# Performance work log

Hardware: AMD Instinct MI355X
Metric: run time of the kernel (lower is better)

Reference implementation:

```python
import jax, jax.numpy as jnp
import numpy as np

NUM_FEATURES = 256
NUM_HEADS = 8
HEAD_SIZE = NUM_FEATURES // NUM_HEADS  # 32
N_AGENTS = 8
B = 32
SEQ = 64


def setup_inputs() -> dict:
    key = jax.random.key(0)
    ks = jax.random.split(key, 6)
    s = 0.02
    x = jax.random.normal(ks[0], (N_AGENTS * B, NUM_FEATURES, SEQ), dtype=jnp.float32)
    Wq = jax.random.normal(ks[1], (NUM_HEADS, NUM_FEATURES, HEAD_SIZE), dtype=jnp.float32) * s
    Wk = jax.random.normal(ks[2], (NUM_HEADS, NUM_FEATURES, HEAD_SIZE), dtype=jnp.float32) * s
    Wv = jax.random.normal(ks[3], (NUM_HEADS, NUM_FEATURES, HEAD_SIZE), dtype=jnp.float32) * s
    Wp = jax.random.normal(ks[4], (NUM_FEATURES, NUM_FEATURES), dtype=jnp.float32) * s
    bp = jnp.zeros((NUM_FEATURES,), dtype=jnp.float32)
    return {"x": x, "Wq": Wq, "Wk": Wk, "Wv": Wv, "Wp": Wp, "bp": bp, "n_agents": N_AGENTS}


def reference(x, Wq, Wk, Wv, Wp, bp, n_agents):
    # x: (n_agents*b, f, h)
    b_total, f, h = x.shape
    b = b_total // n_agents
    # reshape + rearrange 'n b f h -> n b h f'  (t = token axis of length h)
    xs = x.reshape(n_agents, b, f, h).transpose(0, 1, 3, 2)  # (n, b, t, f)
    # All heads at once: per-head linear projections (no bias)
    q = jnp.einsum('nbtf,Hfd->Hnbtd', xs, Wq)
    k = jnp.einsum('nbtf,Hfd->Hnbtd', xs, Wk)
    v = jnp.einsum('nbtf,Hfd->Hnbtd', xs, Wv)
    # all-pairs agent attention: i = key agent, j = query agent
    scale = f ** (-0.5)  # source scales by num_features, not head_size
    scores = jnp.einsum('Hjbtd,Hibsd->Hijbts', q, k) * scale  # (H,n,n,b,t,s)
    attn = jax.nn.softmax(scores, axis=-1)
    # weighted values, then sum over key-agent axis i
    out = jnp.einsum('Hijbts,Hibsd->Hjbtd', attn, v)  # (H,n,b,t,d)
    # concat heads on last dim (head 0 first), matching torch.cat
    y = jnp.moveaxis(out, 0, 3).reshape(n_agents, b, h, f)  # (n,b,t,H*d)
    # output projection (dropout is identity at eval / p=0)
    y = jnp.einsum('nbtf,gf->nbtg', y, Wp) + bp
    # rearrange 'n b h f -> n b f h' then merge agents into batch
    y = y.transpose(0, 1, 3, 2).reshape(n_agents * b, f, h)
    return y
```

## Files before the change

kernel.cpp:

```cpp
#include <hip/hip_runtime.h>

#define F   256
#define T   64
#define NH  8
#define D   32
#define NA  8
#define NBB 32

typedef unsigned short ushortT;
typedef unsigned int   uintT;

typedef short bf16x8 __attribute__((ext_vector_type(8)));
typedef float f32x4  __attribute__((ext_vector_type(4)));

__device__ __forceinline__ float bf2f(ushortT u) {
    union { uintT i; float f; } c; c.i = ((uintT)u) << 16; return c.f;
}
__device__ __forceinline__ ushortT f2bf(float f) {
    union { float f; uintT u; } c; c.f = f;
    uintT u = c.u;
    uintT r = u + 0x7fffu + ((u >> 16) & 1u);
    return (ushortT)(r >> 16);
}

__device__ __forceinline__ int detect_isbf16(const void* xraw) {
    const uintT* w = (const uintT*)xraw;
    int bad = 0;
    for (int k = 0; k < 128; ++k) {
        uintT v = w[k];
        uintT e0 = (v >> 7)  & 0xffu;
        uintT e1 = (v >> 23) & 0xffu;
        bad += (e0 > 131u) + (e1 > 131u);
    }
    return bad == 0 ? 1 : 0;
}

__device__ __forceinline__ ushortT cvt_elem(const void* p, size_t i, bool isbf) {
    return isbf ? ((const ushortT*)p)[i] : f2bf(((const float*)p)[i]);
}

__device__ __forceinline__ void packc(const f32x4 v, float scale, uintT& u0, uintT& u1) {
    u0 = (uintT)f2bf(v[0] * scale) | ((uintT)f2bf(v[1] * scale) << 16);
    u1 = (uintT)f2bf(v[2] * scale) | ((uintT)f2bf(v[3] * scale) << 16);
}

__device__ __forceinline__ bf16x8 build_frag(uintT u0a, uintT u1a, uintT u0b, uintT u1b,
                                             int sl0, int sl1, bool hi) {
    union { uintT u[4]; bf16x8 v; } r;
    uintT x0a = (uintT)__shfl((int)u0a, sl0), x0b = (uintT)__shfl((int)u0b, sl0);
    uintT x1a = (uintT)__shfl((int)u1a, sl0), x1b = (uintT)__shfl((int)u1b, sl0);
    uintT x2a = (uintT)__shfl((int)u0a, sl1), x2b = (uintT)__shfl((int)u0b, sl1);
    uintT x3a = (uintT)__shfl((int)u1a, sl1), x3b = (uintT)__shfl((int)u1b, sl1);
    r.u[0] = hi ? x0b : x0a;
    r.u[1] = hi ? x1b : x1a;
    r.u[2] = hi ? x2b : x2a;
    r.u[3] = hi ? x3b : x3a;
    return r.v;
}

__device__ __forceinline__ int xposU(int t, int f) {
    return t * 256 + ((((f >> 3) ^ (t & 31)) * 8) | (f & 7));
}
#define FRAGPOS(t_, ks_, quad_) \
    ((t_) * 256 + ((((4 * (ks_) + (quad_)) ^ ((t_) & 31)) * 8)))


__global__ __launch_bounds__(256) void wprep_kernel(const void* __restrict__ Wq,
                                                    const void* __restrict__ Wk,
                                                    const void* __restrict__ Wv,
                                                    const void* __restrict__ Wp,
                                                    const void* __restrict__ x,
                                                    ushortT* __restrict__ Wt) {
    __shared__ int sflag;
    if (threadIdx.x == 0) sflag = detect_isbf16(x);
    __syncthreads();
    bool isbf = sflag != 0;

    int base = (blockIdx.x * 256 + threadIdx.x) * 8;
    int cp = base >> 8, f0 = base & 255;

    ushortT tmp[8];
    if (cp < 768) {
        int qkv = cp >> 8, c = cp & 255, hh = c >> 5, d = c & 31;
        const void* W = (qkv == 0) ? Wq : (qkv == 1) ? Wk : Wv;
        #pragma unroll
        for (int jj = 0; jj < 8; ++jj)
            tmp[jj] = cvt_elem(W, (size_t)(hh * F + f0 + jj) * D + d, isbf);
    } else {
        int g = cp - 768;
        #pragma unroll
        for (int jj = 0; jj < 8; ++jj)
            tmp[jj] = cvt_elem(Wp, (size_t)g * F + f0 + jj, isbf);
    }
    *(uint4*)&Wt[base] = *(const uint4*)tmp;
}

template <int NT>
__device__ __forceinline__ void stage_xT(const void* x, int nb, ushortT* xs,
                                         bool isbf, int tid) {
    int t = tid & 63;
    int g0 = tid >> 6;
    const int GP = NT / 64;
    #pragma unroll
    for (int it = 0; it < 64 / GP; ++it) {
        int g = g0 + it * GP;
        float v0, v1, v2, v3;
        if (isbf) {
            const ushortT* xp = (const ushortT*)x + (size_t)nb * (F * T) + (size_t)g * 4 * T + t;
            v0 = bf2f(xp[0]); v1 = bf2f(xp[T]); v2 = bf2f(xp[2 * T]); v3 = bf2f(xp[3 * T]);
        } else {
            const float* xp = (const float*)x + (size_t)nb * (F * T) + (size_t)g * 4 * T + t;
            v0 = xp[0]; v1 = xp[T]; v2 = xp[2 * T]; v3 = xp[3 * T];
        }
        uintT lo = (uintT)f2bf(v0) | ((uintT)f2bf(v1) << 16);
        uintT hi2 = (uintT)f2bf(v2) | ((uintT)f2bf(v3) << 16);
        *(uint2*)&xs[xposU(t & 31, g * 4) + (t >> 5) * 8192] = make_uint2(lo, hi2);
    }
}

__global__ __launch_bounds__(256) void qkv_kernel(const void* __restrict__ x,
                                                  const ushortT* __restrict__ Wt,
                                                  ushortT* __restrict__ Kws,
                                                  ushortT* __restrict__ Vws) {
    int nb = blockIdx.x, half = blockIdx.y;
    __shared__ __align__(16) ushortT xs[T * F];
    __shared__ int sflag;
    int tid = threadIdx.x;
    if (tid == 0) sflag = detect_isbf16(x);
    __syncthreads();
    bool isbf = sflag != 0;
    stage_xT<256>(x, nb, xs, isbf, tid);
    __syncthreads();

    int w = tid >> 6, lane = tid & 63, l15 = lane & 15, quad = lane >> 4;
    int rowbase = 256 + 256 * half + 64 * w;

    f32x4 acc[4][4];
    #pragma unroll
    for (int a = 0; a < 4; ++a)
        #pragma unroll
        for (int c = 0; c < 4; ++c) acc[a][c] = (f32x4){0.f, 0.f, 0.f, 0.f};

    #pragma unroll
    for (int ks = 0; ks < 8; ++ks) {
        bf16x8 Bfr[4];
        #pragma unroll
        for (int nt = 0; nt < 4; ++nt) {
            int t = 16 * nt + l15;
            Bfr[nt] = *(const bf16x8*)&xs[FRAGPOS(t & 31, ks, quad) + (t >> 5) * 8192];
        }
        #pragma unroll
        for (int mt = 0; mt < 4; ++mt) {
            bf16x8 Afr = *(const bf16x8*)(Wt +
                (size_t)(rowbase + 16 * mt + l15) * 256 + ks * 32 + quad * 8);
            #pragma unroll
            for (int nt = 0; nt < 4; ++nt)
                acc[mt][nt] = __builtin_amdgcn_mfma_f32_16x16x32_bf16(Afr, Bfr[nt],
                                                                      acc[mt][nt], 0, 0, 0);
        }
    }

    #pragma unroll
    for (int mt = 0; mt < 4; ++mt) {
        int rel = 64 * w + 16 * mt + 4 * quad;
        int hh = rel >> 5, db = rel & 31;
        #pragma unroll
        for (int nt = 0; nt < 4; ++nt) {
            int t = 16 * nt + l15;
            f32x4 v = acc[mt][nt];
            if (half == 0) {
                ushortT* dst = Kws + ((size_t)(nb * NH + hh) * T + t) * D + db;
                uintT lo = (uintT)f2bf(v[0]) | ((uintT)f2bf(v[1]) << 16);
                uintT hi2 = (uintT)f2bf(v[2]) | ((uintT)f2bf(v[3]) << 16);
                *(uint2*)dst = make_uint2(lo, hi2);
            } else {
                #pragma unroll
                for (int r = 0; r < 4; ++r)
                    Vws[((size_t)(nb * NH + hh) * D + db + r) * T + t] = f2bf(v[r]);
            }
        }
    }
}

__global__ __launch_bounds__(512, 2) void attn_kernel(const void* __restrict__ x,
                                                      const ushortT* __restrict__ Wt,
                                                      const ushortT* __restrict__ Kws,
                                                      const ushortT* __restrict__ Vws,
                                                      const void* __restrict__ bp,
                                                      void* __restrict__ outp) {
    __shared__ __align__(16) ushortT xs[32 * F];
    __shared__ float bpf[F];
    __shared__ int sflag;

    int tid = threadIdx.x;
    int b = blockIdx.x, j = blockIdx.y, tb = blockIdx.z;
    int nbj = j * NBB + b;

    if (tid == 0) sflag = detect_isbf16(x);
    __syncthreads();
    bool isbf = sflag != 0;

    {
        int t = tid & 31, fg = tid >> 5;
        int ta = tb * 32 + t;
        #pragma unroll
        for (int it = 0; it < 4; ++it) {
            int f0 = (fg + 16 * it) * 4;
            float v0, v1, v2, v3;
            if (isbf) {
                const ushortT* xp = (const ushortT*)x + (size_t)nbj * (F * T) +
                                    (size_t)f0 * T + ta;
                v0 = bf2f(xp[0]); v1 = bf2f(xp[T]); v2 = bf2f(xp[2 * T]); v3 = bf2f(xp[3 * T]);
            } else {
                const float* xp = (const float*)x + (size_t)nbj * (F * T) +
                                  (size_t)f0 * T + ta;
                v0 = xp[0]; v1 = xp[T]; v2 = xp[2 * T]; v3 = xp[3 * T];
            }
            uintT lo = (uintT)f2bf(v0) | ((uintT)f2bf(v1) << 16);
            uintT hi2 = (uintT)f2bf(v2) | ((uintT)f2bf(v3) << 16);
            *(uint2*)&xs[xposU(t, f0)] = make_uint2(lo, hi2);
        }
    }
    if (tid < 256)
        bpf[tid] = isbf ? bf2f(((const ushortT*)bp)[tid]) : ((const float*)bp)[tid];
    __syncthreads();

    int h = tid >> 6, lane = tid & 63, l15 = lane & 15, quad = lane >> 4;
    bool hi = quad >= 2;
    int sl0 = l15 + 32 * (quad & 1), sl1 = sl0 + 16;

    bf16x8 qf[2];
    {
        f32x4 qacc[2][2];
        #pragma unroll
        for (int mt = 0; mt < 2; ++mt)
            #pragma unroll
            for (int nt = 0; nt < 2; ++nt) qacc[mt][nt] = (f32x4){0.f, 0.f, 0.f, 0.f};
        #pragma unroll
        for (int ks = 0; ks < 8; ++ks) {
            bf16x8 xf[2];
            #pragma unroll
            for (int nt = 0; nt < 2; ++nt)
                xf[nt] = *(const bf16x8*)&xs[FRAGPOS(16 * nt + l15, ks, quad)];
            #pragma unroll
            for (int mt = 0; mt < 2; ++mt) {
                bf16x8 Aw = *(const bf16x8*)(Wt +
                    (size_t)(32 * h + 16 * mt + l15) * 256 + ks * 32 + quad * 8);
                #pragma unroll
                for (int nt = 0; nt < 2; ++nt)
                    qacc[mt][nt] = __builtin_amdgcn_mfma_f32_16x16x32_bf16(
                        Aw, xf[nt], qacc[mt][nt], 0, 0, 0);
            }
        }
        #pragma unroll
        for (int tt = 0; tt < 2; ++tt) {
            uintT a0, a1, b0, b1;
            packc(qacc[0][tt], 0.0625f, a0, a1);
            packc(qacc[1][tt], 0.0625f, b0, b1);
            qf[tt] = build_frag(a0, a1, b0, b1, sl0, sl1, hi);
        }
    }

    f32x4 oacc[2][2];
    #pragma unroll
    for (int mt = 0; mt < 2; ++mt)
        #pragma unroll
        for (int tt = 0; tt < 2; ++tt) oacc[mt][tt] = (f32x4){0.f, 0.f, 0.f, 0.f};

    for (int i = 0; i < NA; ++i) {
        int nbi = i * NBB + b;
        const ushortT* Kb = Kws + (size_t)(nbi * NH + h) * T * D;
        const ushortT* Vb = Vws + (size_t)(nbi * NH + h) * D * T;

        float psum[2] = {0.f, 0.f};
        f32x4 pv[2][2];
        #pragma unroll
        for (int mt = 0; mt < 2; ++mt)
            #pragma unroll
            for (int tt = 0; tt < 2; ++tt) pv[mt][tt] = (f32x4){0.f, 0.f, 0.f, 0.f};

        #pragma unroll
        for (int kx = 0; kx < 2; ++kx) {
            uintT pu0[2][2], pu1[2][2];
            #pragma unroll
            for (int sp = 0; sp < 2; ++sp) {
                bf16x8 kf = *(const bf16x8*)(Kb + (16 * (2 * kx + sp) + l15) * D + quad * 8);
                #pragma unroll
                for (int tt = 0; tt < 2; ++tt) {
                    f32x4 s4 = __builtin_amdgcn_mfma_f32_16x16x32_bf16(
                        kf, qf[tt], (f32x4){0.f, 0.f, 0.f, 0.f}, 0, 0, 0);
                    #pragma unroll
                    for (int r = 0; r < 4; ++r) {
                        float e = __expf(s4[r]);
                        s4[r] = e;
                        psum[tt] += e;
                    }
                    packc(s4, 1.f, pu0[sp][tt], pu1[sp][tt]);
                }
            }
            bf16x8 vf0 = *(const bf16x8*)(Vb + l15 * T + kx * 32 + quad * 8);
            bf16x8 vf1 = *(const bf16x8*)(Vb + (16 + l15) * T + kx * 32 + quad * 8);
            #pragma unroll
            for (int tt = 0; tt < 2; ++tt) {
                bf16x8 pf = build_frag(pu0[0][tt], pu1[0][tt], pu0[1][tt], pu1[1][tt],
                                       sl0, sl1, hi);
                pv[0][tt] = __builtin_amdgcn_mfma_f32_16x16x32_bf16(
                    vf0, pf, pv[0][tt], 0, 0, 0);
                pv[1][tt] = __builtin_amdgcn_mfma_f32_16x16x32_bf16(
                    vf1, pf, pv[1][tt], 0, 0, 0);
            }
        }

        #pragma unroll
        for (int tt = 0; tt < 2; ++tt) {
            float s = psum[tt];
            s += __shfl_xor(s, 16);
            s += __shfl_xor(s, 32);
            float inv = 1.0f / s;
            #pragma unroll
            for (int mt = 0; mt < 2; ++mt)
                #pragma unroll
                for (int r = 0; r < 4; ++r)
                    oacc[mt][tt][r] = fmaf(inv, pv[mt][tt][r], oacc[mt][tt][r]);
        }
    }

    __syncthreads();
    #pragma unroll
    for (int mt = 0; mt < 2; ++mt)
        #pragma unroll
        for (int tt = 0; tt < 2; ++tt) {
            int t = 16 * tt + l15;
            int cb = 32 * h + 16 * mt + 4 * quad;
            uintT u0, u1;
            packc(oacc[mt][tt], 1.f, u0, u1);
            *(uint2*)&xs[xposU(t, cb)] = make_uint2(u0, u1);
        }
    __syncthreads();

    f32x4 cacc[2][2];
    #pragma unroll
    for (int a = 0; a < 2; ++a)
        #pragma unroll
        for (int c = 0; c < 2; ++c) cacc[a][c] = (f32x4){0.f, 0.f, 0.f, 0.f};

    #pragma unroll
    for (int ks = 0; ks < 8; ++ks) {
        bf16x8 yb[2];
        #pragma unroll
        for (int nt = 0; nt < 2; ++nt)
            yb[nt] = *(const bf16x8*)&xs[FRAGPOS(16 * nt + l15, ks, quad)];
        #pragma unroll
        for (int m2 = 0; m2 < 2; ++m2) {
            int g = 16 * (2 * h + m2) + l15;
            bf16x8 wf = *(const bf16x8*)(Wt + (size_t)(768 + g) * 256 + ks * 32 + quad * 8);
            #pragma unroll
            for (int nt = 0; nt < 2; ++nt)
                cacc[m2][nt] = __builtin_amdgcn_mfma_f32_16x16x32_bf16(
                    wf, yb[nt], cacc[m2][nt], 0, 0, 0);
        }
    }

    #pragma unroll
    for (int m2 = 0; m2 < 2; ++m2)
        #pragma unroll
        for (int nt = 0; nt < 2; ++nt) {
            int t = tb * 32 + 16 * nt + l15;
            #pragma unroll
            for (int r = 0; r < 4; ++r) {
                int g = 16 * (2 * h + m2) + 4 * quad + r;
                float val = cacc[m2][nt][r] + bpf[g];
                if (isbf)
                    ((ushortT*)outp)[(size_t)nbj * F * T + g * T + t] = f2bf(val);
                else
                    ((float*)outp)[(size_t)nbj * F * T + g * T + t] = val;
            }
        }
}

__device__ __forceinline__ float tof(ushortT u) { return bf2f(u); }
__device__ __forceinline__ float tof(float f)   { return f; }

__device__ __forceinline__ void stage_x(const void* x, size_t nb, ushortT* sX,
                                        bool isbf, int tid) {
    if (isbf) {
        const int4* xg = (const int4*)((const ushortT*)x + nb * (F * T));
        int4* xl = (int4*)sX;
        for (int kk = tid; kk < F * T / 8; kk += 512) xl[kk] = xg[kk];
    } else {
        const float4* xg = (const float4*)((const float*)x + nb * (F * T));
        for (int kk = tid; kk < F * T / 4; kk += 512) {
            float4 v = xg[kk];
            int o = kk * 4;
            sX[o + 0] = f2bf(v.x); sX[o + 1] = f2bf(v.y);
            sX[o + 2] = f2bf(v.z); sX[o + 3] = f2bf(v.w);
        }
    }
}

template <typename WT>
__device__ __forceinline__ void q_proj(const WT* __restrict__ W, const ushortT* sX,
                                       ushortT* dst, int c, int t0) {
    float acc[32];
    #pragma unroll
    for (int m = 0; m < 32; ++m) acc[m] = 0.f;
    for (int f = 0; f < F; ++f) {
        float w = tof(W[f * D]);
        const ushortT* xr = &sX[f * T + t0];
        #pragma unroll
        for (int m = 0; m < 32; ++m) acc[m] = fmaf(bf2f(xr[m]), w, acc[m]);
    }
    #pragma unroll
    for (int m = 0; m < 32; ++m) dst[(t0 + m) * F + c] = f2bf(acc[m]);
}

template <typename WT>
__device__ __forceinline__ void kv_proj(const WT* __restrict__ WK, const WT* __restrict__ WV,
                                        const ushortT* sX, ushortT* sK, ushortT* sV,
                                        int c, int t0) {
    float ak[32], av[32];
    #pragma unroll
    for (int m = 0; m < 32; ++m) { ak[m] = 0.f; av[m] = 0.f; }
    for (int f = 0; f < F; ++f) {
        float wk = tof(WK[f * D]);
        float wv = tof(WV[f * D]);
        const ushortT* xr = &sX[f * T + t0];
        #pragma unroll
        for (int m = 0; m < 32; ++m) {
            float xv = bf2f(xr[m]);
            ak[m] = fmaf(xv, wk, ak[m]);
            av[m] = fmaf(xv, wv, av[m]);
        }
    }
    #pragma unroll
    for (int m = 0; m < 32; ++m) {
        sK[(t0 + m) * F + c] = f2bf(ak[m]);
        sV[(t0 + m) * F + c] = f2bf(av[m]);
    }
}

__global__ __launch_bounds__(512) void fused_kernel(const void* __restrict__ x,
                                                    const void* __restrict__ Wq,
                                                    const void* __restrict__ Wk,
                                                    const void* __restrict__ Wv,
                                                    const void* __restrict__ Wp,
                                                    const void* __restrict__ bp,
                                                    void* __restrict__ outp) {
    __shared__ __align__(16) char smem[98304];
    __shared__ int sflag;
    ushortT* sX = (ushortT*)smem;
    ushortT* sK = (ushortT*)(smem + 32768);
    ushortT* sV = (ushortT*)(smem + 65536);
    float*   sO = (float*)smem;

    int tid = threadIdx.x;
    int b = blockIdx.x, j = blockIdx.y;
    size_t nbj = (size_t)j * NBB + b;

    if (tid == 0) sflag = detect_isbf16(x);
    __syncthreads();
    bool isbf = sflag != 0;

    stage_x(x, nbj, sX, isbf, tid);
    __syncthreads();

    int c = tid & 255, t0 = (tid >> 8) * 32;
    int hc = c >> 5, dc = c & 31;
    if (isbf) q_proj((const ushortT*)Wq + (size_t)hc * F * D + dc, sX, sK, c, t0);
    else      q_proj((const float*)Wq   + (size_t)hc * F * D + dc, sX, sK, c, t0);
    __syncthreads();

    int h = tid >> 6, t = tid & 63;
    float q[32], o[32];
    #pragma unroll
    for (int dd = 0; dd < 32; ++dd) { q[dd] = bf2f(sK[t * F + h * D + dd]); o[dd] = 0.f; }

    for (int i = 0; i < NA; ++i) {
        __syncthreads();
        stage_x(x, (size_t)(i * NBB + b), sX, isbf, tid);
        __syncthreads();
        if (isbf) kv_proj((const ushortT*)Wk + (size_t)hc * F * D + dc,
                          (const ushortT*)Wv + (size_t)hc * F * D + dc, sX, sK, sV, c, t0);
        else      kv_proj((const float*)Wk   + (size_t)hc * F * D + dc,
                          (const float*)Wv   + (size_t)hc * F * D + dc, sX, sK, sV, c, t0);
        __syncthreads();
        float l = 0.f;
        float oi[32];
        #pragma unroll
        for (int dd = 0; dd < 32; ++dd) oi[dd] = 0.f;
        for (int s = 0; s < T; ++s) {
            const ushortT* kr = &sK[s * F + h * D];
            float dot = 0.f;
            #pragma unroll
            for (int dd = 0; dd < 32; ++dd) dot = fmaf(q[dd], bf2f(kr[dd]), dot);
            float e = __expf(dot * 0.0625f);
            l += e;
            const ushortT* vr = &sV[s * F + h * D];
            #pragma unroll
            for (int dd = 0; dd < 32; ++dd) oi[dd] = fmaf(e, bf2f(vr[dd]), oi[dd]);
        }
        float inv = 1.0f / l;
        #pragma unroll
        for (int dd = 0; dd < 32; ++dd) o[dd] = fmaf(inv, oi[dd], o[dd]);
    }
    __syncthreads();

    #pragma unroll
    for (int dd = 0; dd < 32; ++dd) sO[(h * D + dd) * T + t] = o[dd];
    __syncthreads();

    {
        int g = tid >> 1, te0 = (tid & 1) * 32;
        float acc[32];
        #pragma unroll
        for (int m = 0; m < 32; ++m) acc[m] = 0.f;
        if (isbf) {
            const ushortT* Wrow = (const ushortT*)Wp + (size_t)g * F;
            for (int cc = 0; cc < F; ++cc) {
                float w = bf2f(Wrow[cc]);
                const float* yr = &sO[cc * T + te0];
                #pragma unroll
                for (int m = 0; m < 32; ++m) acc[m] = fmaf(yr[m], w, acc[m]);
            }
        } else {
            const float* Wrow = (const float*)Wp + (size_t)g * F;
            for (int cc = 0; cc < F; ++cc) {
                float w = Wrow[cc];
                const float* yr = &sO[cc * T + te0];
                #pragma unroll
                for (int m = 0; m < 32; ++m) acc[m] = fmaf(yr[m], w, acc[m]);
            }
        }
        float bias = isbf ? bf2f(((const ushortT*)bp)[g]) : ((const float*)bp)[g];
        if (isbf) {
            ushortT* ob = (ushortT*)outp + nbj * F * T + g * T + te0;
            #pragma unroll
            for (int m = 0; m < 32; ++m) ob[m] = f2bf(acc[m] + bias);
        } else {
            float* ob = (float*)outp + nbj * F * T + g * T + te0;
            #pragma unroll
            for (int m = 0; m < 32; ++m) ob[m] = acc[m] + bias;
        }
    }
}

extern "C" void kernel_launch(void* const* d_in, const int* in_sizes, int n_in,
                              void* d_out, int out_size, void* d_ws, size_t ws_size,
                              hipStream_t stream) {
    const void* x  = d_in[0];
    const void* Wq = d_in[1];
    const void* Wk = d_in[2];
    const void* Wv = d_in[3];
    const void* Wp = d_in[4];
    const void* bp = d_in[5];

    const size_t needA = 17301504;

    if (ws_size >= needA) {
        char* ws = (char*)d_ws;
        ushortT* Wt  = (ushortT*)(ws + 0);
        ushortT* Kws = (ushortT*)(ws + 524288);
        ushortT* Vws = (ushortT*)(ws + 8912896);

        wprep_kernel<<<dim3(128),      dim3(256), 0, stream>>>(Wq, Wk, Wv, Wp, x, Wt);
        qkv_kernel  <<<dim3(256, 2),   dim3(256), 0, stream>>>(x, Wt, Kws, Vws);
        attn_kernel <<<dim3(32, 8, 2), dim3(512), 0, stream>>>(x, Wt, Kws, Vws, bp, d_out);
    } else {
        fused_kernel<<<dim3(32, 8), dim3(512), 0, stream>>>(x, Wq, Wk, Wv, Wp, bp, d_out);
    }
}
```

Measured before the change: 150.5 us.

## Split QKV and attention grids finer and use cheaper packed bf16 conversion

The QKV projection grid doubles to four parts per sample, with each wave computing 32 rows instead of 64. The attention kernel now processes 16 query tokens per block instead of 32 and launches twice as many blocks, with smaller shared memory and a higher occupancy hint. The float-to-bf16 packing now uses a round-half-up add plus a byte perm instead of round-to-nearest-even, which slightly changes rounding. More blocks each restage x and reload K/V, so global traffic rises in exchange for more parallelism and fewer registers per thread.

After: 182.0 us. +20.9%, slower.

```diff
diff --git a/kernel.cpp b/kernel.cpp
--- a/kernel.cpp
+++ b/kernel.cpp
@@ -21,6 +21,14 @@
     uintT u = c.u;
     uintT r = u + 0x7fffu + ((u >> 16) & 1u);
     return (ushortT)(r >> 16);
+}
+__device__ __forceinline__ uintT asu(float f) {
+    union { float f; uintT u; } c; c.f = f; return c.u;
+}
+__device__ __forceinline__ uintT pk2bf(float a, float b) {
+    uintT ua = asu(a) + 0x8000u;
+    uintT ub = asu(b) + 0x8000u;
+    return __builtin_amdgcn_perm(ub, ua, 0x07060302u);
 }
 
 __device__ __forceinline__ int detect_isbf16(const void* xraw) {
@@ -40,8 +48,8 @@
 }
 
 __device__ __forceinline__ void packc(const f32x4 v, float scale, uintT& u0, uintT& u1) {
-    u0 = (uintT)f2bf(v[0] * scale) | ((uintT)f2bf(v[1] * scale) << 16);
-    u1 = (uintT)f2bf(v[2] * scale) | ((uintT)f2bf(v[3] * scale) << 16);
+    u0 = pk2bf(v[0] * scale, v[1] * scale);
+    u1 = pk2bf(v[2] * scale, v[3] * scale);
 }
 
 __device__ __forceinline__ bf16x8 build_frag(uintT u0a, uintT u1a, uintT u0b, uintT u1b,
@@ -63,6 +71,11 @@
 }
 #define FRAGPOS(t_, ks_, quad_) \
     ((t_) * 256 + ((((4 * (ks_) + (quad_)) ^ ((t_) & 31)) * 8)))
+__device__ __forceinline__ int xposU16(int t, int f) {
+    return t * 256 + ((((f >> 3) ^ t) & 31) * 8) + (f & 7);
+}
+#define FRAGPOS16(t_, ks_, quad_) \
+    ((t_) * 256 + ((((4 * (ks_) + (quad_)) ^ (t_)) & 31) * 8))
 
 
 __global__ __launch_bounds__(256) void wprep_kernel(const void* __restrict__ Wq,
@@ -95,15 +108,13 @@
     *(uint4*)&Wt[base] = *(const uint4*)tmp;
 }
 
-template <int NT>
 __device__ __forceinline__ void stage_xT(const void* x, int nb, ushortT* xs,
                                          bool isbf, int tid) {
     int t = tid & 63;
     int g0 = tid >> 6;
-    const int GP = NT / 64;
-    #pragma unroll
-    for (int it = 0; it < 64 / GP; ++it) {
-        int g = g0 + it * GP;
+    #pragma unroll
+    for (int it = 0; it < 16; ++it) {
+        int g = g0 + it * 4;
         float v0, v1, v2, v3;
         if (isbf) {
             const ushortT* xp = (const ushortT*)x + (size_t)nb * (F * T) + (size_t)g * 4 * T + t;
@@ -112,32 +123,32 @@
             const float* xp = (const float*)x + (size_t)nb * (F * T) + (size_t)g * 4 * T + t;
             v0 = xp[0]; v1 = xp[T]; v2 = xp[2 * T]; v3 = xp[3 * T];
         }
-        uintT lo = (uintT)f2bf(v0) | ((uintT)f2bf(v1) << 16);
-        uintT hi2 = (uintT)f2bf(v2) | ((uintT)f2bf(v3) << 16);
-        *(uint2*)&xs[xposU(t & 31, g * 4) + (t >> 5) * 8192] = make_uint2(lo, hi2);
-    }
-}
-
-__global__ __launch_bounds__(256) void qkv_kernel(const void* __restrict__ x,
-                                                  const ushortT* __restrict__ Wt,
-                                                  ushortT* __restrict__ Kws,
-                                                  ushortT* __restrict__ Vws) {
-    int nb = blockIdx.x, half = blockIdx.y;
+        *(uint2*)&xs[xposU(t & 31, g * 4) + (t >> 5) * 8192] =
+            make_uint2(pk2bf(v0, v1), pk2bf(v2, v3));
+    }
+}
+
+__global__ __launch_bounds__(256, 4) void qkv_kernel(const void* __restrict__ x,
+                                                     const ushortT* __restrict__ Wt,
+                                                     ushortT* __restrict__ Kws,
+                                                     ushortT* __restrict__ Vws) {
+    int nb = blockIdx.x, part = blockIdx.y;
+    int is_v = part >> 1, sub = part & 1;
     __shared__ __align__(16) ushortT xs[T * F];
     __shared__ int sflag;
     int tid = threadIdx.x;
     if (tid == 0) sflag = detect_isbf16(x);
     __syncthreads();
     bool isbf = sflag != 0;
-    stage_xT<256>(x, nb, xs, isbf, tid);
+    stage_xT(x, nb, xs, isbf, tid);
     __syncthreads();
 
     int w = tid >> 6, lane = tid & 63, l15 = lane & 15, quad = lane >> 4;
-    int rowbase = 256 + 256 * half + 64 * w;
-
-    f32x4 acc[4][4];
-    #pragma unroll
-    for (int a = 0; a < 4; ++a)
+    int rowbase = 256 + 256 * is_v + 128 * sub + 32 * w;
+
+    f32x4 acc[2][4];
+    #pragma unroll
+    for (int a = 0; a < 2; ++a)
         #pragma unroll
         for (int c = 0; c < 4; ++c) acc[a][c] = (f32x4){0.f, 0.f, 0.f, 0.f};
 
@@ -150,7 +161,7 @@
             Bfr[nt] = *(const bf16x8*)&xs[FRAGPOS(t & 31, ks, quad) + (t >> 5) * 8192];
         }
         #pragma unroll
-        for (int mt = 0; mt < 4; ++mt) {
+        for (int mt = 0; mt < 2; ++mt) {
             bf16x8 Afr = *(const bf16x8*)(Wt +
                 (size_t)(rowbase + 16 * mt + l15) * 256 + ks * 32 + quad * 8);
             #pragma unroll
@@ -161,18 +172,16 @@
     }
 
     #pragma unroll
-    for (int mt = 0; mt < 4; ++mt) {
-        int rel = 64 * w + 16 * mt + 4 * quad;
+    for (int mt = 0; mt < 2; ++mt) {
+        int rel = 128 * sub + 32 * w + 16 * mt + 4 * quad;
         int hh = rel >> 5, db = rel & 31;
         #pragma unroll
         for (int nt = 0; nt < 4; ++nt) {
             int t = 16 * nt + l15;
             f32x4 v = acc[mt][nt];
-            if (half == 0) {
+            if (is_v == 0) {
                 ushortT* dst = Kws + ((size_t)(nb * NH + hh) * T + t) * D + db;
-                uintT lo = (uintT)f2bf(v[0]) | ((uintT)f2bf(v[1]) << 16);
-                uintT hi2 = (uintT)f2bf(v[2]) | ((uintT)f2bf(v[3]) << 16);
-                *(uint2*)dst = make_uint2(lo, hi2);
+                *(uint2*)dst = make_uint2(pk2bf(v[0], v[1]), pk2bf(v[2], v[3]));
             } else {
                 #pragma unroll
                 for (int r = 0; r < 4; ++r)
@@ -182,13 +191,13 @@
     }
 }
 
-__global__ __launch_bounds__(512, 2) void attn_kernel(const void* __restrict__ x,
+__global__ __launch_bounds__(512, 4) void attn_kernel(const void* __restrict__ x,
                                                       const ushortT* __restrict__ Wt,
                                                       const ushortT* __restrict__ Kws,
                                                       const ushortT* __restrict__ Vws,
                                                       const void* __restrict__ bp,
                                                       void* __restrict__ outp) {
-    __shared__ __align__(16) ushortT xs[32 * F];
+    __shared__ __align__(16) ushortT xs[16 * F];
     __shared__ float bpf[F];
     __shared__ int sflag;
 
@@ -201,11 +210,11 @@
     bool isbf = sflag != 0;
 
     {
-        int t = tid & 31, fg = tid >> 5;
-        int ta = tb * 32 + t;
-        #pragma unroll
-        for (int it = 0; it < 4; ++it) {
-            int f0 = (fg + 16 * it) * 4;
+        int t = tid & 15, fg = tid >> 4;
+        int ta = tb * 16 + t;
+        #pragma unroll
+        for (int it = 0; it < 2; ++it) {
+            int f0 = (fg + 32 * it) * 4;
             float v0, v1, v2, v3;
             if (isbf) {
                 const ushortT* xp = (const ushortT*)x + (size_t)nbj * (F * T) +
@@ -216,9 +225,7 @@
                                   (size_t)f0 * T + ta;
                 v0 = xp[0]; v1 = xp[T]; v2 = xp[2 * T]; v3 = xp[3 * T];
             }
-            uintT lo = (uintT)f2bf(v0) | ((uintT)f2bf(v1) << 16);
-            uintT hi2 = (uintT)f2bf(v2) | ((uintT)f2bf(v3) << 16);
-            *(uint2*)&xs[xposU(t, f0)] = make_uint2(lo, hi2);
+            *(uint2*)&xs[xposU16(t, f0)] = make_uint2(pk2bf(v0, v1), pk2bf(v2, v3));
         }
     }
     if (tid < 256)
@@ -229,153 +236,113 @@
     bool hi = quad >= 2;
     int sl0 = l15 + 32 * (quad & 1), sl1 = sl0 + 16;
 
-    bf16x8 qf[2];
+    bf16x8 qf;
     {
-        f32x4 qacc[2][2];
-        #pragma unroll
-        for (int mt = 0; mt < 2; ++mt)
-            #pragma unroll
-            for (int nt = 0; nt < 2; ++nt) qacc[mt][nt] = (f32x4){0.f, 0.f, 0.f, 0.f};
+        f32x4 qacc[2];
+        qacc[0] = (f32x4){0.f, 0.f, 0.f, 0.f};
+        qacc[1] = (f32x4){0.f, 0.f, 0.f, 0.f};
         #pragma unroll
         for (int ks = 0; ks < 8; ++ks) {
-            bf16x8 xf[2];
-            #pragma unroll
-            for (int nt = 0; nt < 2; ++nt)
-                xf[nt] = *(const bf16x8*)&xs[FRAGPOS(16 * nt + l15, ks, quad)];
+            bf16x8 xf = *(const bf16x8*)&xs[FRAGPOS16(l15, ks, quad)];
             #pragma unroll
             for (int mt = 0; mt < 2; ++mt) {
                 bf16x8 Aw = *(const bf16x8*)(Wt +
                     (size_t)(32 * h + 16 * mt + l15) * 256 + ks * 32 + quad * 8);
-                #pragma unroll
-                for (int nt = 0; nt < 2; ++nt)
-                    qacc[mt][nt] = __builtin_amdgcn_mfma_f32_16x16x32_bf16(
-                        Aw, xf[nt], qacc[mt][nt], 0, 0, 0);
+                qacc[mt] = __builtin_amdgcn_mfma_f32_16x16x32_bf16(
+                    Aw, xf, qacc[mt], 0, 0, 0);
             }
         }
-        #pragma unroll
-        for (int tt = 0; tt < 2; ++tt) {
-            uintT a0, a1, b0, b1;
-            packc(qacc[0][tt], 0.0625f, a0, a1);
-            packc(qacc[1][tt], 0.0625f, b0, b1);
-            qf[tt] = build_frag(a0, a1, b0, b1, sl0, sl1, hi);
-        }
-    }
-
-    f32x4 oacc[2][2];
-    #pragma unroll
-    for (int mt = 0; mt < 2; ++mt)
-        #pragma unroll
-        for (int tt = 0; tt < 2; ++tt) oacc[mt][tt] = (f32x4){0.f, 0.f, 0.f, 0.f};
+        uintT a0, a1, b0, b1;
+        packc(qacc[0], 0.0625f, a0, a1);
+        packc(qacc[1], 0.0625f, b0, b1);
+        qf = build_frag(a0, a1, b0, b1, sl0, sl1, hi);
+    }
+
+    f32x4 oacc[2];
+    oacc[0] = (f32x4){0.f, 0.f, 0.f, 0.f};
+    oacc[1] = (f32x4){0.f, 0.f, 0.f, 0.f};
 
     for (int i = 0; i < NA; ++i) {
         int nbi = i * NBB + b;
         const ushortT* Kb = Kws + (size_t)(nbi * NH + h) * T * D;
         const ushortT* Vb = Vws + (size_t)(nbi * NH + h) * D * T;
 
-        float psum[2] = {0.f, 0.f};
-        f32x4 pv[2][2];
-        #pragma unroll
-        for (int mt = 0; mt < 2; ++mt)
-            #pragma unroll
-            for (int tt = 0; tt < 2; ++tt) pv[mt][tt] = (f32x4){0.f, 0.f, 0.f, 0.f};
+        float psum = 0.f;
+        f32x4 pv[2];
+        pv[0] = (f32x4){0.f, 0.f, 0.f, 0.f};
+        pv[1] = (f32x4){0.f, 0.f, 0.f, 0.f};
 
         #pragma unroll
         for (int kx = 0; kx < 2; ++kx) {
-            uintT pu0[2][2], pu1[2][2];
+            uintT pu0[2], pu1[2];
             #pragma unroll
             for (int sp = 0; sp < 2; ++sp) {
                 bf16x8 kf = *(const bf16x8*)(Kb + (16 * (2 * kx + sp) + l15) * D + quad * 8);
+                f32x4 s4 = __builtin_amdgcn_mfma_f32_16x16x32_bf16(
+                    kf, qf, (f32x4){0.f, 0.f, 0.f, 0.f}, 0, 0, 0);
                 #pragma unroll
-                for (int tt = 0; tt < 2; ++tt) {
-                    f32x4 s4 = __builtin_amdgcn_mfma_f32_16x16x32_bf16(
-                        kf, qf[tt], (f32x4){0.f, 0.f, 0.f, 0.f}, 0, 0, 0);
-                    #pragma unroll
-                    for (int r = 0; r < 4; ++r) {
-                        float e = __expf(s4[r]);
-                        s4[r] = e;
-                        psum[tt] += e;
-                    }
-                    packc(s4, 1.f, pu0[sp][tt], pu1[sp][tt]);
+                for (int r = 0; r < 4; ++r) {
+                    float e = __expf(s4[r]);
+                    s4[r] = e;
+                    psum += e;
                 }
+                packc(s4, 1.f, pu0[sp], pu1[sp]);
             }
+            bf16x8 pf = build_frag(pu0[0], pu1[0], pu0[1], pu1[1], sl0, sl1, hi);
             bf16x8 vf0 = *(const bf16x8*)(Vb + l15 * T + kx * 32 + quad * 8);
             bf16x8 vf1 = *(const bf16x8*)(Vb + (16 + l15) * T + kx * 32 + quad * 8);
-            #pragma unroll
-            for (int tt = 0; tt < 2; ++tt) {
-                bf16x8 pf = build_frag(pu0[0][tt], pu1[0][tt], pu0[1][tt], pu1[1][tt],
-                                       sl0, sl1, hi);
-                pv[0][tt] = __builtin_amdgcn_mfma_f32_16x16x32_bf16(
-                    vf0, pf, pv[0][tt], 0, 0, 0);
-                pv[1][tt] = __builtin_amdgcn_mfma_f32_16x16x32_bf16(
-                    vf1, pf, pv[1][tt], 0, 0, 0);
-            }
-        }
-
-        #pragma unroll
-        for (int tt = 0; tt < 2; ++tt) {
-            float s = psum[tt];
-            s += __shfl_xor(s, 16);
-            s += __shfl_xor(s, 32);
-            float inv = 1.0f / s;
-            #pragma unroll
-            for (int mt = 0; mt < 2; ++mt)
-                #pragma unroll
-                for (int r = 0; r < 4; ++r)
-                    oacc[mt][tt][r] = fmaf(inv, pv[mt][tt][r], oacc[mt][tt][r]);
-        }
-    }
-
-    __syncthreads();
-    #pragma unroll
-    for (int mt = 0; mt < 2; ++mt)
-        #pragma unroll
-        for (int tt = 0; tt < 2; ++tt) {
-            int t = 16 * tt + l15;
-            int cb = 32 * h + 16 * mt + 4 * quad;
-            uintT u0, u1;
-            packc(oacc[mt][tt], 1.f, u0, u1);
-            *(uint2*)&xs[xposU(t, cb)] = make_uint2(u0, u1);
-        }
-    __syncthreads();
-
-    f32x4 cacc[2][2];
-    #pragma unroll
-    for (int a = 0; a < 2; ++a)
-        #pragma unroll
-        for (int c = 0; c < 2; ++c) cacc[a][c] = (f32x4){0.f, 0.f, 0.f, 0.f};
+            pv[0] = __builtin_amdgcn_mfma_f32_16x16x32_bf16(vf0, pf, pv[0], 0, 0, 0);
+            pv[1] = __builtin_amdgcn_mfma_f32_16x16x32_bf16(vf1, pf, pv[1], 0, 0, 0);
+        }
+
+        psum += __shfl_xor(psum, 16);
+        psum += __shfl_xor(psum, 32);
+        float inv = 1.0f / psum;
+        #pragma unroll
+        for (int mt = 0; mt < 2; ++mt)
+            #pragma unroll
+            for (int r = 0; r < 4; ++r)
+                oacc[mt][r] = fmaf(inv, pv[mt][r], oacc[mt][r]);
+    }
+
+    __syncthreads();
+    #pragma unroll
+    for (int mt = 0; mt < 2; ++mt) {
+        int cb = 32 * h + 16 * mt + 4 * quad;
+        uintT u0, u1;
+        packc(oacc[mt], 1.f, u0, u1);
+        *(uint2*)&xs[xposU16(l15, cb)] = make_uint2(u0, u1);
+    }
+    __syncthreads();
+
+    f32x4 cacc[2];
+    cacc[0] = (f32x4){0.f, 0.f, 0.f, 0.f};
+    cacc[1] = (f32x4){0.f, 0.f, 0.f, 0.f};
 
     #pragma unroll
     for (int ks = 0; ks < 8; ++ks) {
-        bf16x8 yb[2];
-        #pragma unroll
-        for (int nt = 0; nt < 2; ++nt)
-            yb[nt] = *(const bf16x8*)&xs[FRAGPOS(16 * nt + l15, ks, quad)];
+        bf16x8 yb = *(const bf16x8*)&xs[FRAGPOS16(l15, ks, quad)];
         #pragma unroll
         for (int m2 = 0; m2 < 2; ++m2) {
             int g = 16 * (2 * h + m2) + l15;
             bf16x8 wf = *(const bf16x8*)(Wt + (size_t)(768 + g) * 256 + ks * 32 + quad * 8);
-            #pragma unroll
-            for (int nt = 0; nt < 2; ++nt)
-                cacc[m2][nt] = __builtin_amdgcn_mfma_f32_16x16x32_bf16(
-                    wf, yb[nt], cacc[m2][nt], 0, 0, 0);
-        }
-    }
-
-    #pragma unroll
-    for (int m2 = 0; m2 < 2; ++m2)
-        #pragma unroll
-        for (int nt = 0; nt < 2; ++nt) {
-            int t = tb * 32 + 16 * nt + l15;
-            #pragma unroll
-            for (int r = 0; r < 4; ++r) {
-                int g = 16 * (2 * h + m2) + 4 * quad + r;
-                float val = cacc[m2][nt][r] + bpf[g];
-                if (isbf)
-                    ((ushortT*)outp)[(size_t)nbj * F * T + g * T + t] = f2bf(val);
-                else
-                    ((float*)outp)[(size_t)nbj * F * T + g * T + t] = val;
-            }
-        }
+            cacc[m2] = __builtin_amdgcn_mfma_f32_16x16x32_bf16(wf, yb, cacc[m2], 0, 0, 0);
+        }
+    }
+
+    #pragma unroll
+    for (int m2 = 0; m2 < 2; ++m2) {
+        int t = tb * 16 + l15;
+        #pragma unroll
+        for (int r = 0; r < 4; ++r) {
+            int g = 16 * (2 * h + m2) + 4 * quad + r;
+            float val = cacc[m2][r] + bpf[g];
+            if (isbf)
+                ((ushortT*)outp)[(size_t)nbj * F * T + g * T + t] = f2bf(val);
+            else
+                ((float*)outp)[(size_t)nbj * F * T + g * T + t] = val;
+        }
+    }
 }
 
 __device__ __forceinline__ float tof(ushortT u) { return bf2f(u); }
@@ -563,8 +530,8 @@
         ushortT* Vws = (ushortT*)(ws + 8912896);
 
         wprep_kernel<<<dim3(128),      dim3(256), 0, stream>>>(Wq, Wk, Wv, Wp, x, Wt);
-        qkv_kernel  <<<dim3(256, 2),   dim3(256), 0, stream>>>(x, Wt, Kws, Vws);
-        attn_kernel <<<dim3(32, 8, 2), dim3(512), 0, stream>>>(x, Wt, Kws, Vws, bp, d_out);
+        qkv_kernel  <<<dim3(256, 4),   dim3(256), 0, stream>>>(x, Wt, Kws, Vws);
+        attn_kernel <<<dim3(32, 8, 4), dim3(512), 0, stream>>>(x, Wt, Kws, Vws, bp, d_out);
     } else {
         fused_kernel<<<dim3(32, 8), dim3(512), 0, stream>>>(x, Wq, Wk, Wv, Wp, bp, d_out);
     }
```
